# Kernel tuning notes

Measured on AMD Instinct MI355X. Metric: run time of the kernel, lower is better.

The kernel has to match this reference:

```python
import jax, jax.numpy as jnp
import numpy as np

DIM = 512
HEADS = 8
DIM_HEAD = 64
INNER = HEADS * DIM_HEAD  # 512


def setup_inputs() -> dict:
    key = jax.random.key(0)
    k1, k2, k3, k4 = jax.random.split(key, 4)
    x = jax.random.normal(k1, (2, 4096, DIM), dtype=jnp.float32)
    w_qkv = jax.random.normal(k2, (DIM, INNER * 3), dtype=jnp.float32) * (DIM ** -0.5)
    w_out = jax.random.normal(k3, (INNER, DIM), dtype=jnp.float32) * (INNER ** -0.5)
    b_out = jnp.zeros((DIM,), dtype=jnp.float32)
    temperature = jnp.asarray(np.log(DIM_HEAD ** -0.5), dtype=jnp.float32)
    return {"x": x, "w_qkv": w_qkv, "w_out": w_out, "b_out": b_out,
            "temperature": temperature}


def reference(x, w_qkv, w_out, b_out, temperature):
    b, n, _ = x.shape
    qkv = jnp.einsum('bnd,de->bne', x, w_qkv)            # [b,n,3*inner]
    q, k, v = jnp.split(qkv, 3, axis=-1)
    # 'b n (h d) -> b h n d'
    def to_heads(t):
        return t.reshape(b, n, HEADS, DIM_HEAD).transpose(0, 2, 1, 3)
    q, k, v = map(to_heads, (q, k, v))
    scale = jnp.exp(temperature)
    dots = jnp.einsum('bhid,bhjd->bhij', q, k) * scale   # [b,h,n,n]
    mask_value = -jnp.asarray(np.finfo(np.float32).max, dtype=dots.dtype)
    eye = jnp.eye(n, dtype=bool)
    dots = jnp.where(eye, mask_value, dots)
    attn = jax.nn.softmax(dots, axis=-1)
    out = jnp.einsum('bhij,bhjd->bhid', attn, v)         # [b,h,n,d]
    out = out.transpose(0, 2, 1, 3).reshape(b, n, INNER)  # 'b h n d -> b n (h d)'
    return jnp.einsum('bni,io->bno', out, w_out) + b_out
```

## Files before the change

kernel.cpp:

```cpp
#include <hip/hip_runtime.h>

typedef __bf16 bf16x8 __attribute__((ext_vector_type(8)));
typedef float  f32x4  __attribute__((ext_vector_type(4)));
typedef unsigned short u16;
typedef unsigned int   u32;

#define MFMA16(a,b,c) __builtin_amdgcn_mfma_f32_16x16x32_bf16((a),(b),(c),0,0,0)

__device__ __forceinline__ u16 f2bf(float f){
    u32 u = __builtin_bit_cast(u32, f);
    u += 0x7FFFu + ((u >> 16) & 1u);
    return (u16)(u >> 16);
}

__device__ __forceinline__ u32 cvt_pk_bf16(float lo, float hi){
    u32 r;
    asm("v_cvt_pk_bf16_f32 %0, %1, %2" : "=v"(r) : "v"(lo), "v"(hi));
    return r;
}

__device__ __forceinline__ float max3f(float a, float b, float c){
    return fmaxf(fmaxf(a, b), c);
}

typedef __attribute__((address_space(3))) u32 lds32_t;
typedef __attribute__((address_space(1))) u32 glb32_t;

__device__ __forceinline__ void gll16(const u16* g, u16* l){
    __builtin_amdgcn_global_load_lds((const glb32_t*)g, (lds32_t*)l, 16, 0, 0);
}

__global__ __launch_bounds__(256) void cvt_x_kernel(const float* __restrict__ in,
                                                    u16* __restrict__ out, int n8){
    int i = blockIdx.x * 256 + threadIdx.x;
    if (i >= n8) return;
    const float4* p = (const float4*)in + (size_t)i * 2;
    float4 a = p[0], b = p[1];
    u16 r[8] = { f2bf(a.x), f2bf(a.y), f2bf(a.z), f2bf(a.w),
                 f2bf(b.x), f2bf(b.y), f2bf(b.z), f2bf(b.w) };
    *((uint4*)out + i) = *(const uint4*)r;
}

__global__ __launch_bounds__(256) void tcvt_kernel(const float* __restrict__ in,
                                                   u16* __restrict__ out, int R, int C){
    __shared__ float tile[32][33];
    int c0 = blockIdx.x * 32, r0 = blockIdx.y * 32;
    int tx = threadIdx.x & 31, ty = threadIdx.x >> 5;
    #pragma unroll
    for (int i = 0; i < 32; i += 8)
        tile[ty + i][tx] = in[(size_t)(r0 + ty + i) * C + c0 + tx];
    __syncthreads();
    #pragma unroll
    for (int i = 0; i < 32; i += 8)
        out[(size_t)(c0 + ty + i) * R + r0 + tx] = f2bf(tile[tx][ty + i]);
}

__device__ __forceinline__ void gemm_core(const u16* __restrict__ A, const u16* __restrict__ Bt,
                                          int brow, int bcol, u16* ldsA, u16* ldsB,
                                          f32x4 acc[4][4]){
    const int t = threadIdx.x;
    const int lane = t & 63, wave = t >> 6;
    const int l16 = lane & 15, lg = lane >> 4;
    const int wrow = (wave & 1) << 6, wcol = (wave >> 1) << 6;

    for (int ks = 0; ks < 8; ++ks){
        if (ks) __syncthreads();
        #pragma unroll
        for (int iss = 0; iss < 4; ++iss){
            int chunk = iss * 256 + t;
            int row = chunk >> 3, c = chunk & 7;
            int sw = (c ^ (row & 7)) << 3;
            gll16(A  + (size_t)(brow + row) * 512 + ks * 64 + sw,
                  ldsA + (size_t)(iss * 256 + wave * 64) * 8);
            gll16(Bt + (size_t)(bcol + row) * 512 + ks * 64 + sw,
                  ldsB + (size_t)(iss * 256 + wave * 64) * 8);
        }
        __syncthreads();
        #pragma unroll
        for (int kc = 0; kc < 2; ++kc){
            bf16x8 af[4], bfr[4];
            #pragma unroll
            for (int m = 0; m < 4; ++m){
                int r = wrow + 16 * m + l16;
                af[m] = *(const bf16x8*)(ldsA + r * 64 + (((kc * 4 + lg) ^ (l16 & 7)) << 3));
            }
            #pragma unroll
            for (int n = 0; n < 4; ++n){
                int r = wcol + 16 * n + l16;
                bfr[n] = *(const bf16x8*)(ldsB + r * 64 + (((kc * 4 + lg) ^ (l16 & 7)) << 3));
            }
            #pragma unroll
            for (int m = 0; m < 4; ++m)
                #pragma unroll
                for (int n = 0; n < 4; ++n)
                    acc[m][n] = MFMA16(af[m], bfr[n], acc[m][n]);
        }
    }
}

__global__ __launch_bounds__(256) void gemm_qkv_kernel(const u16* __restrict__ A, const u16* __restrict__ Bt,
                                                       u16* __restrict__ qws, u16* __restrict__ kws,
                                                       u16* __restrict__ vtws,
                                                       const float* __restrict__ temp){
    __shared__ u16 ldsA[128 * 64];
    __shared__ u16 ldsB[128 * 64];
    const f32x4 vzero = {0.f, 0.f, 0.f, 0.f};
    f32x4 acc[4][4];
    #pragma unroll
    for (int m = 0; m < 4; ++m)
        #pragma unroll
        for (int n = 0; n < 4; ++n) acc[m][n] = vzero;

    int brow = blockIdx.x * 128, bcol = blockIdx.y * 128;
    gemm_core(A, Bt, brow, bcol, ldsA, ldsB, acc);

    const int t = threadIdx.x, lane = t & 63, wave = t >> 6;
    const int l16 = lane & 15, lg = lane >> 4;
    const int wrow = (wave & 1) << 6, wcol = (wave >> 1) << 6;
    const int s = bcol >> 9;

    if (s < 2){
        u16* dst = (s == 0) ? qws : kws;
        float qs = (s == 0) ? (__expf(temp[0]) * 1.44269504f) : 1.0f;
        #pragma unroll
        for (int n = 0; n < 4; ++n){
            int e = (bcol & 511) + wcol + 16 * n + l16;
            int h = e >> 6, d = e & 63;
            #pragma unroll
            for (int m = 0; m < 4; ++m)
                #pragma unroll
                for (int r = 0; r < 4; ++r){
                    int mg = brow + wrow + 16 * m + 4 * lg + r;
                    int b = mg >> 12, nn = mg & 4095;
                    dst[(((size_t)(b * 8 + h) * 4096 + nn) << 6) + d] = f2bf(acc[m][n][r] * qs);
                }
        }
    } else {
        #pragma unroll
        for (int n = 0; n < 4; ++n){
            int e = (bcol & 511) + wcol + 16 * n + l16;
            int h = e >> 6, d = e & 63;
            #pragma unroll
            for (int m = 0; m < 4; ++m)
                #pragma unroll
                for (int r = 0; r < 4; ++r){
                    int mg = brow + wrow + 16 * m + 4 * lg + r;
                    int b = mg >> 12, nn = mg & 4095;
                    vtws[((size_t)((b * 8 + h) * 64 + d) << 12) + nn] = f2bf(acc[m][n][r]);
                }
        }
    }
}

__global__ __launch_bounds__(256) void attn_kernel(const u16* __restrict__ q, const u16* __restrict__ k,
                                                   const u16* __restrict__ vt, u16* __restrict__ aout){
    __shared__ u16 Kl[64 * 64];
    __shared__ u16 Vl[64 * 64];
    __shared__ u16 Pl[4][16 * 72];
    const int bid = blockIdx.x;
    const int qt = bid & 63, bh = bid >> 6;
    const int t = threadIdx.x, lane = t & 63, wave = t >> 6;
    const int l16 = lane & 15, lg = lane >> 4;

    const int qrow = qt * 64 + wave * 16 + l16;
    const u16* qb = q + (((size_t)bh * 4096 + qrow) << 6);
    bf16x8 qa[2];
    qa[0] = *(const bf16x8*)(qb + (lg << 3));
    qa[1] = *(const bf16x8*)(qb + 32 + (lg << 3));

    const uint4 ow = {0x3F803F80u, 0x3F803F80u, 0x3F803F80u, 0x3F803F80u};
    const bf16x8 ones = __builtin_bit_cast(bf16x8, ow);

    const f32x4 vzero = {0.f, 0.f, 0.f, 0.f};
    f32x4 o[4];
    f32x4 o4 = vzero;
    #pragma unroll
    for (int i = 0; i < 4; ++i) o[i] = vzero;
    float mv = -INFINITY;

    for (int kb = 0; kb < 4096; kb += 64){
        __syncthreads();
        #pragma unroll
        for (int iss = 0; iss < 2; ++iss){
            int chunk = iss * 256 + t;
            int row = chunk >> 3, c = chunk & 7;
            int sw = (c ^ (row & 7)) << 3;
            gll16(k  + (((size_t)bh * 4096 + kb + row) << 6) + sw,
                  Kl + (iss * 256 + wave * 64) * 8);
            gll16(vt + ((size_t)(bh * 64 + row) << 12) + kb + sw,
                  Vl + (iss * 256 + wave * 64) * 8);
        }
        __syncthreads();

        f32x4 s[4];
        __builtin_amdgcn_s_setprio(1);
        #pragma unroll
        for (int fc = 0; fc < 4; ++fc){
            s[fc] = vzero;
            #pragma unroll
            for (int dc = 0; dc < 2; ++dc){
                bf16x8 kf = *(const bf16x8*)(Kl + (16 * fc + l16) * 64 +
                                             (((dc * 4 + lg) ^ (l16 & 7)) << 3));
            s[fc] = MFMA16(kf, qa[dc], s[fc]);
            }
        }
        __builtin_amdgcn_s_setprio(0);
        if (kb == qt * 64){
            int dd = wave * 16 + l16;
            #pragma unroll
            for (int fc = 0; fc < 4; ++fc)
                #pragma unroll
                for (int r = 0; r < 4; ++r)
                    if (dd == fc * 16 + 4 * lg + r) s[fc][r] = -1e30f;
        }
        float g0 = max3f(s[0][0], s[0][1], s[0][2]);
        float g1 = max3f(s[0][3], s[1][0], s[1][1]);
        float g2 = max3f(s[1][2], s[1][3], s[2][0]);
        float g3 = max3f(s[2][1], s[2][2], s[2][3]);
        float g4 = max3f(s[3][0], s[3][1], s[3][2]);
        float pm = fmaxf(max3f(max3f(g0, g1, g2), g3, g4), s[3][3]);
        pm = fmaxf(pm, __shfl_xor(pm, 16));
        pm = fmaxf(pm, __shfl_xor(pm, 32));
        if (__any(pm > mv + 8.0f)){
            float mn = fmaxf(mv, pm);
            float al = __builtin_amdgcn_exp2f(mv - mn);
            mv = mn;
            o4 *= al;
            #pragma unroll
            for (int dn = 0; dn < 4; ++dn)
                #pragma unroll
                for (int r = 0; r < 4; ++r) o[dn][r] *= al;
        }
        #pragma unroll
        for (int fc = 0; fc < 4; ++fc){
            float p0 = __builtin_amdgcn_exp2f(s[fc][0] - mv);
            float p1 = __builtin_amdgcn_exp2f(s[fc][1] - mv);
            float p2 = __builtin_amdgcn_exp2f(s[fc][2] - mv);
            float p3 = __builtin_amdgcn_exp2f(s[fc][3] - mv);
            uint2 w;
            w.x = cvt_pk_bf16(p0, p1);
            w.y = cvt_pk_bf16(p2, p3);
            *(uint2*)&Pl[wave][l16 * 72 + 16 * fc + 4 * lg] = w;
        }
        __builtin_amdgcn_s_setprio(1);
        #pragma unroll
        for (int kc = 0; kc < 2; ++kc){
            bf16x8 pa = *(const bf16x8*)(&Pl[wave][l16 * 72 + kc * 32 + lg * 8]);
            o4 = MFMA16(ones, pa, o4);
            #pragma unroll
            for (int dn = 0; dn < 4; ++dn){
                bf16x8 vf = *(const bf16x8*)(Vl + (16 * dn + l16) * 64 +
                                             (((kc * 4 + lg) ^ (l16 & 7)) << 3));
                o[dn] = MFMA16(vf, pa, o[dn]);
            }
        }
        __builtin_amdgcn_s_setprio(0);
    }
    const int b = bh >> 3, h = bh & 7;
    const float inv = __builtin_amdgcn_rcpf(o4[0]);
    const int n = qt * 64 + wave * 16 + l16;
    size_t base = ((size_t)b * 4096 + n) * 512 + h * 64;
    #pragma unroll
    for (int dn = 0; dn < 4; ++dn){
        u16 e0 = f2bf(o[dn][0] * inv), e1 = f2bf(o[dn][1] * inv);
        u16 e2 = f2bf(o[dn][2] * inv), e3 = f2bf(o[dn][3] * inv);
        uint2 w;
        w.x = (u32)e0 | ((u32)e1 << 16);
        w.y = (u32)e2 | ((u32)e3 << 16);
        *(uint2*)&aout[base + dn * 16 + lg * 4] = w;
    }
}

__global__ __launch_bounds__(256) void gemm_out_kernel(const u16* __restrict__ A, const u16* __restrict__ Bt,
                                                       const float* __restrict__ bias,
                                                       float* __restrict__ out){
    __shared__ u16 ldsA[128 * 64];
    __shared__ u16 ldsB[128 * 64];
    const f32x4 vzero = {0.f, 0.f, 0.f, 0.f};
    f32x4 acc[4][4];
    #pragma unroll
    for (int m = 0; m < 4; ++m)
        #pragma unroll
        for (int n = 0; n < 4; ++n) acc[m][n] = vzero;

    int brow = blockIdx.x * 128, bcol = blockIdx.y * 128;
    gemm_core(A, Bt, brow, bcol, ldsA, ldsB, acc);

    const int t = threadIdx.x, lane = t & 63, wave = t >> 6;
    const int l16 = lane & 15, lg = lane >> 4;
    const int wrow = (wave & 1) << 6, wcol = (wave >> 1) << 6;
    #pragma unroll
    for (int n = 0; n < 4; ++n){
        int e = bcol + wcol + 16 * n + l16;
        float bv = bias[e];
        #pragma unroll
        for (int m = 0; m < 4; ++m)
            #pragma unroll
            for (int r = 0; r < 4; ++r){
                int mg = brow + wrow + 16 * m + 4 * lg + r;
                out[(size_t)mg * 512 + e] = acc[m][n][r] + bv;
            }
    }
}

extern "C" void kernel_launch(void* const* d_in, const int* in_sizes, int n_in,
                              void* d_out, int out_size, void* d_ws, size_t ws_size,
                              hipStream_t stream){
    (void)in_sizes; (void)n_in; (void)out_size; (void)ws_size;
    const float* x     = (const float*)d_in[0];
    const float* w_qkv = (const float*)d_in[1];
    const float* w_out = (const float*)d_in[2];
    const float* b_out = (const float*)d_in[3];
    const float* temp  = (const float*)d_in[4];
    float* out = (float*)d_out;

    u16* ws   = (u16*)d_ws;
    u16* xbf  = ws;
    u16* wqt  = xbf + 8192 * 512;
    u16* wot  = wqt + 1536 * 512;
    u16* qws  = wot + 512 * 512;
    u16* kws  = qws + 16 * 4096 * 64;
    u16* vtws = kws + 16 * 4096 * 64;
    u16* aout = xbf;

    cvt_x_kernel<<<2048, 256, 0, stream>>>(x, xbf, 8192 * 512 / 8);
    tcvt_kernel<<<dim3(48, 16), 256, 0, stream>>>(w_qkv, wqt, 512, 1536);
    tcvt_kernel<<<dim3(16, 16), 256, 0, stream>>>(w_out, wot, 512, 512);
    gemm_qkv_kernel<<<dim3(64, 12), 256, 0, stream>>>(xbf, wqt, qws, kws, vtws, temp);
    attn_kernel<<<1024, 256, 0, stream>>>(qws, kws, vtws, aout);
    gemm_out_kernel<<<dim3(64, 4), 256, 0, stream>>>(aout, wot, b_out, out);
}
```

Measured before the change: 170.2 us.

## Prefetch next K/V tile into registers and remap block order

Replaces the direct global-to-LDS loads with register prefetch: the next K/V tile is loaded into registers while the current tile's QK^T, softmax and PV run, then written to LDS between barriers. The block index is also permuted so consecutive launched blocks spread across batch-heads in strides of 128, which changes cache locality of K/V across concurrently running blocks. The prefetch adds 16 registers per thread for the tile and keeps two barriers per iteration. It overlaps global latency with compute instead of stalling on each tile load.

```diff
diff --git a/kernel.cpp b/kernel.cpp
--- a/kernel.cpp
+++ b/kernel.cpp
@@ -157,10 +157,29 @@
     __shared__ u16 Kl[64 * 64];
     __shared__ u16 Vl[64 * 64];
     __shared__ u16 Pl[4][16 * 72];
-    const int bid = blockIdx.x;
+    const int bid0 = blockIdx.x;
+    const int bid = (bid0 & 7) * 128 + (bid0 >> 3);
     const int qt = bid & 63, bh = bid >> 6;
     const int t = threadIdx.x, lane = t & 63, wave = t >> 6;
     const int l16 = lane & 15, lg = lane >> 4;
+
+    const int row0 = t >> 3,        sw0 = (((t & 7)        ^ (row0 & 7)) << 3);
+    const int row1 = (256 + t) >> 3, sw1 = ((((256 + t) & 7) ^ (row1 & 7)) << 3);
+    const u16* kbase = k  + ((size_t)bh << 18);
+    const u16* vbase = vt + ((size_t)bh << 18);
+    uint4 kr0, kr1, vr0, vr1;
+    auto load_regs = [&](int kb){
+        kr0 = *(const uint4*)(kbase + ((kb + row0) << 6) + sw0);
+        kr1 = *(const uint4*)(kbase + ((kb + row1) << 6) + sw1);
+        vr0 = *(const uint4*)(vbase + (row0 << 12) + kb + sw0);
+        vr1 = *(const uint4*)(vbase + (row1 << 12) + kb + sw1);
+    };
+    auto write_lds = [&](){
+        *(uint4*)(Kl + t * 8)         = kr0;
+        *(uint4*)(Kl + (256 + t) * 8) = kr1;
+        *(uint4*)(Vl + t * 8)         = vr0;
+        *(uint4*)(Vl + (256 + t) * 8) = vr1;
+    };
 
     const int qrow = qt * 64 + wave * 16 + l16;
     const u16* qb = q + (((size_t)bh * 4096 + qrow) << 6);
@@ -178,19 +197,13 @@
     for (int i = 0; i < 4; ++i) o[i] = vzero;
     float mv = -INFINITY;
 
-    for (int kb = 0; kb < 4096; kb += 64){
-        __syncthreads();
-        #pragma unroll
-        for (int iss = 0; iss < 2; ++iss){
-            int chunk = iss * 256 + t;
-            int row = chunk >> 3, c = chunk & 7;
-            int sw = (c ^ (row & 7)) << 3;
-            gll16(k  + (((size_t)bh * 4096 + kb + row) << 6) + sw,
-                  Kl + (iss * 256 + wave * 64) * 8);
-            gll16(vt + ((size_t)(bh * 64 + row) << 12) + kb + sw,
-                  Vl + (iss * 256 + wave * 64) * 8);
-        }
-        __syncthreads();
+    load_regs(0);
+    write_lds();
+    __syncthreads();
+
+    for (int it = 0; it < 64; ++it){
+        const int kb = it << 6;
+        if (it < 63) load_regs(kb + 64);
 
         f32x4 s[4];
         __builtin_amdgcn_s_setprio(1);
@@ -201,7 +214,7 @@
             for (int dc = 0; dc < 2; ++dc){
                 bf16x8 kf = *(const bf16x8*)(Kl + (16 * fc + l16) * 64 +
                                              (((dc * 4 + lg) ^ (l16 & 7)) << 3));
-            s[fc] = MFMA16(kf, qa[dc], s[fc]);
+                s[fc] = MFMA16(kf, qa[dc], s[fc]);
             }
         }
         __builtin_amdgcn_s_setprio(0);
@@ -255,6 +268,12 @@
             }
         }
         __builtin_amdgcn_s_setprio(0);
+
+        if (it < 63){
+            __syncthreads();
+            write_lds();
+            __syncthreads();
+        }
     }
     const int b = bh >> 3, h = bh & 7;
     const float inv = __builtin_amdgcn_rcpf(o4[0]);
```

Result: no change. 168.2 us (-1.2%).
